# Optimization experiments

Hardware: AMD Instinct MI355X
Metric: run time of the kernel (lower is better)

## Reference

```python
import jax, jax.numpy as jnp
import numpy as np

B, N, F = 4096, 128, 3
EPS = 1e-5


def _bn(x, g, b):
    # BatchNorm1d(element_num) on [B, N, C]: channels are dim 1 (the N elements);
    # training-mode stats over dims (0, 2), biased variance (torch default).
    m = x.mean(axis=(0, 2), keepdims=True)
    v = ((x - m) ** 2).mean(axis=(0, 2), keepdims=True)
    return (x - m) / jnp.sqrt(v + EPS) * g[None, :, None] + b[None, :, None]


def _rel(x, W, bvec, psi, phi, wr):
    # f'_i = wr/N * sum_{j != i} (psi*phi * <x_i, x_j>) * relu(unary(x_j))
    n = x.shape[1]
    U = jax.nn.relu(jnp.einsum('bnd,ed->bne', x, W) + bvec)       # [B,N,D]
    S = (psi * phi) * jnp.einsum('bnd,bmd->bnm', x, x)            # [B,N,N]
    S = S * (1.0 - jnp.eye(n, dtype=x.dtype))                     # exclude j == i
    return wr * jnp.einsum('bnm,bmd->bnd', S, U) / n


def setup_inputs() -> dict:
    key = jax.random.key(0)
    ks = iter(jax.random.split(key, 64))
    d1, d2 = 2 * F, 4 * F  # 6, 12

    def w(shape, s=0.1):
        return (jax.random.normal(next(ks), shape, dtype=jnp.float32) * s)

    def scalar():
        return jax.random.uniform(next(ks), (), dtype=jnp.float32)

    inp = {
        'x': jax.random.normal(next(ks), (B, N, F), dtype=jnp.float32),
        'fc1_w': w((d1, F)), 'fc1_b': w((d1,)),
        'bn1_g': jnp.ones((N,), jnp.float32), 'bn1_b': jnp.zeros((N,), jnp.float32),
        'fc2_w': w((d2, d1)), 'fc2_b': w((d2,)),
        'bn2_g': jnp.ones((N,), jnp.float32), 'bn2_b': jnp.zeros((N,), jnp.float32),
        'fc3_w': w((d2, d2)), 'fc3_b': w((d2,)),
        'u1_w': w((d2, d2)), 'u1_b': w((d2,)), 'ps1': scalar(), 'ph1': scalar(), 'wr1': scalar(),
        'u2_w': w((d2, d2)), 'u2_b': w((d2,)), 'ps2': scalar(), 'ph2': scalar(), 'wr2': scalar(),
        'u3_w': w((d2, d2)), 'u3_b': w((d2,)), 'ps3': scalar(), 'ph3': scalar(), 'wr3': scalar(),
        'u4_w': w((d2, d2)), 'u4_b': w((d2,)), 'ps4': scalar(), 'ph4': scalar(), 'wr4': scalar(),
        'fc4_w': w((d1, d2)), 'fc4_b': w((d1,)),
        'bn4_g': jnp.ones((N,), jnp.float32), 'bn4_b': jnp.zeros((N,), jnp.float32),
        'fc5_w': w((F, d1)), 'fc5_b': w((F,)),
        'fc6_w': w((1, F)), 'fc6_b': w((1,)),
        'fc7_w': w((F - 1, F)), 'fc7_b': w((F - 1,)),
        'fc8_w': w((1, F)), 'fc8_b': w((1,)),
    }
    return inp


def reference(x, fc1_w, fc1_b, bn1_g, bn1_b, fc2_w, fc2_b, bn2_g, bn2_b,
              fc3_w, fc3_b,
              u1_w, u1_b, ps1, ph1, wr1,
              u2_w, u2_b, ps2, ph2, wr2,
              u3_w, u3_b, ps3, ph3, wr3,
              u4_w, u4_b, ps4, ph4, wr4,
              fc4_w, fc4_b, bn4_g, bn4_b,
              fc5_w, fc5_b, fc6_w, fc6_b, fc7_w, fc7_b, fc8_w, fc8_b):
    h = jax.nn.relu(_bn(jnp.einsum('bnf,ef->bne', x, fc1_w) + fc1_b, bn1_g, bn1_b))
    h = jax.nn.relu(_bn(jnp.einsum('bnf,ef->bne', h, fc2_w) + fc2_b, bn2_g, bn2_b))
    h = jax.nn.sigmoid(jnp.einsum('bnf,ef->bne', h, fc3_w) + fc3_b)
    h = _rel(h, u1_w, u1_b, ps1, ph1, wr1)
    h = _rel(h, u2_w, u2_b, ps2, ph2, wr2)
    h = _rel(h, u3_w, u3_b, ps3, ph3, wr3)
    h = _rel(h, u4_w, u4_b, ps4, ph4, wr4)
    h = jax.nn.relu(_bn(jnp.einsum('bnf,ef->bne', h, fc4_w) + fc4_b, bn4_g, bn4_b))
    h = jax.nn.relu(jnp.einsum('bnf,ef->bne', h, fc5_w) + fc5_b)
    cls = jnp.einsum('bnf,ef->bne', h, fc6_w) + fc6_b          # [B,N,1]
    geo = jnp.einsum('bnf,ef->bne', h, fc7_w) + fc7_b          # [B,N,F-1]
    res = jnp.concatenate([cls, geo], axis=2)                   # [B,N,F]
    pres = res.max(axis=1)                                      # MaxPool1d over all N -> [B,F]
    pred = jax.nn.sigmoid(pres @ fc8_w.T + fc8_b)               # [B,1]
    return pred
```

## Files before the change

### kernel.cpp

```cpp
#include <hip/hip_runtime.h>
#include <hip/hip_fp16.h>
#include <hip/hip_cooperative_groups.h>

namespace cg = cooperative_groups;

#define BB 4096
#define NN 128
#define EPS 1e-5f

#define S1 0
#define S2 2048
#define S4 4096
#define A4_OFF 6144

static __device__ __forceinline__ float sigmoidf_(float z){
  return 1.f/(1.f+__expf(-z));
}
static __device__ __forceinline__ float2 h2f2_(unsigned u){
  __half2 h = *reinterpret_cast<__half2*>(&u);
  return __half22float2(h);
}

static __device__ __forceinline__ float fdot2_(unsigned a, unsigned b, float c){
#if defined(__has_builtin)
#if __has_builtin(__builtin_amdgcn_fdot2)
  typedef _Float16 h2v __attribute__((ext_vector_type(2)));
  h2v av = *reinterpret_cast<h2v*>(&a);
  h2v bv = *reinterpret_cast<h2v*>(&b);
  return __builtin_amdgcn_fdot2(av, bv, c, false);
#else
  float2 af = h2f2_(a), bf = h2f2_(b);
  return fmaf(af.y, bf.y, fmaf(af.x, bf.x, c));
#endif
#else
  float2 af = h2f2_(a), bf = h2f2_(b);
  return fmaf(af.y, bf.y, fmaf(af.x, bf.x, c));
#endif
}

__global__ __launch_bounds__(256, 4) void kf(
  const float* __restrict__ x,
  const float* __restrict__ w1, const float* __restrict__ b1,
  const float* __restrict__ g1, const float* __restrict__ bb1,
  const float* __restrict__ w2, const float* __restrict__ b2,
  const float* __restrict__ g2, const float* __restrict__ bb2,
  const float* __restrict__ w3, const float* __restrict__ b3,
  const float* __restrict__ u1w, const float* __restrict__ u1b,
  const float* __restrict__ ps1, const float* __restrict__ ph1, const float* __restrict__ wr1,
  const float* __restrict__ u2w, const float* __restrict__ u2b,
  const float* __restrict__ ps2, const float* __restrict__ ph2, const float* __restrict__ wr2,
  const float* __restrict__ u3w, const float* __restrict__ u3b,
  const float* __restrict__ ps3, const float* __restrict__ ph3, const float* __restrict__ wr3,
  const float* __restrict__ u4w, const float* __restrict__ u4b,
  const float* __restrict__ ps4, const float* __restrict__ ph4, const float* __restrict__ wr4,
  const float* __restrict__ w4, const float* __restrict__ b4,
  const float* __restrict__ g4, const float* __restrict__ bb4,
  const float* __restrict__ w5, const float* __restrict__ b5,
  const float* __restrict__ w6, const float* __restrict__ b6,
  const float* __restrict__ w7, const float* __restrict__ b7,
  const float* __restrict__ w8, const float* __restrict__ b8,
  float* __restrict__ st, float* __restrict__ out)
{
  cg::grid_group grid = cg::this_grid();
  __shared__ float lds[4][1536];
  const int t = threadIdx.x;
  const int wave = t >> 6, lane = t & 63;
  const int b = blockIdx.x*4 + wave;
  const int r0 = lane*2, r1 = r0+1;
  const int shadow = (blockIdx.x & 7)*256;
  unsigned* Xp = (unsigned*)&lds[wave][0];
  unsigned* Up = (unsigned*)&lds[wave][768];

  const float2* xr = (const float2*)(x + ((size_t)b*128 + r0)*3);
  float2 c0=xr[0], c1=xr[1], c2=xr[2];
  const float xa0=c0.x, xa1=c0.y, xa2=c1.x;
  const float xb0=c1.y, xb1=c2.x, xb2=c2.y;

  float a6a[6], a6b[6];
  {
    float s0=0.f,q0=0.f,s1v=0.f,q1=0.f;
    #pragma unroll
    for (int e=0;e<6;e++){
      float va = fmaf(xa0,w1[e*3+0], fmaf(xa1,w1[e*3+1], fmaf(xa2,w1[e*3+2], b1[e])));
      float vb = fmaf(xb0,w1[e*3+0], fmaf(xb1,w1[e*3+1], fmaf(xb2,w1[e*3+2], b1[e])));
      a6a[e]=va; a6b[e]=vb;
      s0+=va; q0=fmaf(va,va,q0);
      s1v+=vb; q1=fmaf(vb,vb,q1);
    }
    lds[wave][r0]=s0; lds[wave][r1]=s1v;
    lds[wave][128+r0]=q0; lds[wave][128+r1]=q1;
    __syncthreads();
    atomicAdd(&st[S1 + shadow + t], lds[0][t]+lds[1][t]+lds[2][t]+lds[3][t]);
  }
  grid.sync();

  float z0[12], z1[12];
  {
    float sa=0.f,qa=0.f,sb=0.f,qb=0.f;
    #pragma unroll
    for (int c=0;c<8;c++){
      sa+=st[S1+c*256+r0]; qa+=st[S1+c*256+128+r0];
      sb+=st[S1+c*256+r1]; qb+=st[S1+c*256+128+r1];
    }
    const float inv1 = 1.f/(BB*6);
    float m=sa*inv1, v=qa*inv1-m*m;
    const float sA0=g1[r0]*rsqrtf(v+EPS), hA0=bb1[r0]-m*sA0;
    m=sb*inv1; v=qb*inv1-m*m;
    const float sA1=g1[r1]*rsqrtf(v+EPS), hA1=bb1[r1]-m*sA1;

    float h0[6], h1[6];
    #pragma unroll
    for (int e=0;e<6;e++){
      h0[e]=fmaxf(fmaf(a6a[e],sA0,hA0),0.f);
      h1[e]=fmaxf(fmaf(a6b[e],sA1,hA1),0.f);
    }
    float s0=0.f,q0=0.f,s1v=0.f,q1=0.f;
    #pragma unroll
    for (int d=0;d<12;d++){
      float za=b2[d], zb=b2[d];
      #pragma unroll
      for (int e=0;e<6;e++){ za=fmaf(h0[e],w2[d*6+e],za); zb=fmaf(h1[e],w2[d*6+e],zb); }
      z0[d]=za; z1[d]=zb;
      s0+=za; q0=fmaf(za,za,q0);
      s1v+=zb; q1=fmaf(zb,zb,q1);
    }
    lds[wave][r0]=s0; lds[wave][r1]=s1v;
    lds[wave][128+r0]=q0; lds[wave][128+r1]=q1;
    __syncthreads();
    atomicAdd(&st[S2 + shadow + t], lds[0][t]+lds[1][t]+lds[2][t]+lds[3][t]);
  }
  grid.sync();

  float X0[12], X1[12];
  {
    float sa=0.f,qa=0.f,sb=0.f,qb=0.f;
    #pragma unroll
    for (int c=0;c<8;c++){
      sa+=st[S2+c*256+r0]; qa+=st[S2+c*256+128+r0];
      sb+=st[S2+c*256+r1]; qb+=st[S2+c*256+128+r1];
    }
    const float inv2 = 1.f/(BB*12);
    float m=sa*inv2, v=qa*inv2-m*m;
    const float sB0=g2[r0]*rsqrtf(v+EPS), hB0=bb2[r0]-m*sB0;
    m=sb*inv2; v=qb*inv2-m*m;
    const float sB1=g2[r1]*rsqrtf(v+EPS), hB1=bb2[r1]-m*sB1;

    float h0[12], h1[12];
    #pragma unroll
    for (int d=0;d<12;d++){
      h0[d]=fmaxf(fmaf(z0[d],sB0,hB0),0.f);
      h1[d]=fmaxf(fmaf(z1[d],sB1,hB1),0.f);
    }
    #pragma unroll
    for (int d=0;d<12;d++){
      float za=b3[d], zb=b3[d];
      #pragma unroll
      for (int e=0;e<12;e++){ za=fmaf(h0[e],w3[d*12+e],za); zb=fmaf(h1[e],w3[d*12+e],zb); }
      X0[d]=sigmoidf_(za); X1[d]=sigmoidf_(zb);
    }
  }

  const float* UW[4]  = {u1w,u2w,u3w,u4w};
  const float* UBv[4] = {u1b,u2b,u3b,u4b};
  const float cf[4] = {
    wr1[0]*ps1[0]*ph1[0]*(1.f/128.f),
    wr2[0]*ps2[0]*ph2[0]*(1.f/128.f),
    wr3[0]*ps3[0]*ph3[0]*(1.f/128.f),
    wr4[0]*ps4[0]*ph4[0]*(1.f/128.f)
  };

  const int g = lane>>4;
  int kc = lane & 15; if (kc>11) kc=11;

  #pragma unroll
  for (int l=0;l<4;l++){
    const float* uw = UW[l];
    const float* ub = UBv[l];
    const float coef = cf[l];
    float Y0[12], Y1[12];
    {
      float U0[12], U1[12];
      #pragma unroll
      for (int d=0;d<12;d++){
        float za=ub[d], zb=ub[d];
        #pragma unroll
        for (int e=0;e<12;e++){ za=fmaf(X0[e],uw[d*12+e],za); zb=fmaf(X1[e],uw[d*12+e],zb); }
        U0[d]=fmaxf(za,0.f); U1[d]=fmaxf(zb,0.f);
      }
      float q0=0.f, q1=0.f;
      #pragma unroll
      for (int e=0;e<12;e++){ q0=fmaf(X0[e],X0[e],q0); q1=fmaf(X1[e],X1[e],q1); }
      __half2 hp[12], up[12];
      #pragma unroll
      for (int e=0;e<12;e++){
        hp[e] = __floats2half2_rn(X0[e],X1[e]);
        up[e] = __floats2half2_rn(U0[e],U1[e]);
      }
      {
        const uint4* hpv = (const uint4*)hp;
        const uint4* upv = (const uint4*)up;
        uint4* xw  = (uint4*)(Xp + lane*12);
        uint4* uwp = (uint4*)(Up + lane*12);
        xw[0]=hpv[0]; xw[1]=hpv[1]; xw[2]=hpv[2];
        uwp[0]=upv[0]; uwp[1]=upv[1]; uwp[2]=upv[2];
      }
      const float q0c = coef*q0, q1c = coef*q1;
      #pragma unroll
      for (int d=0;d<12;d++){ Y0[d] = -q0c*U0[d]; Y1[d] = -q1c*U1[d]; }
    }

    float mp[12];
    #pragma unroll
    for (int d=0;d<12;d++) mp[d]=0.f;
    #pragma unroll
    for (int i=0;i<16;i++){
      const int p = (g<<4) | ((i+g)&15);
      const unsigned xv2 = Xp[p*12 + kc];
      const uint4* urow = (const uint4*)(Up + p*12);
      uint4 ua=urow[0], ub4=urow[1], uc=urow[2];
      mp[0]=fdot2_(xv2, ua.x, mp[0]);  mp[1]=fdot2_(xv2, ua.y, mp[1]);
      mp[2]=fdot2_(xv2, ua.z, mp[2]);  mp[3]=fdot2_(xv2, ua.w, mp[3]);
      mp[4]=fdot2_(xv2, ub4.x, mp[4]); mp[5]=fdot2_(xv2, ub4.y, mp[5]);
      mp[6]=fdot2_(xv2, ub4.z, mp[6]); mp[7]=fdot2_(xv2, ub4.w, mp[7]);
      mp[8]=fdot2_(xv2, uc.x, mp[8]);  mp[9]=fdot2_(xv2, uc.y, mp[9]);
      mp[10]=fdot2_(xv2, uc.z, mp[10]); mp[11]=fdot2_(xv2, uc.w, mp[11]);
    }
    #pragma unroll
    for (int d=0;d<12;d++) mp[d] += __shfl_xor(mp[d], 16, 64);
    #pragma unroll
    for (int d=0;d<12;d++) mp[d] += __shfl_xor(mp[d], 32, 64);
    #pragma unroll
    for (int d=0;d<12;d++) mp[d] *= coef;

    #pragma unroll
    for (int k=0;k<12;k++){
      const float xa = X0[k], xb = X1[k];
      #pragma unroll
      for (int d=0;d<12;d++){
        const float mv = __int_as_float(__builtin_amdgcn_readlane(__float_as_int(mp[d]), k));
        Y0[d]=fmaf(xa,mv,Y0[d]); Y1[d]=fmaf(xb,mv,Y1[d]);
      }
    }
    #pragma unroll
    for (int d=0;d<12;d++){ X0[d]=Y0[d]; X1[d]=Y1[d]; }
  }

  float z4a[6], z4b[6];
  {
    float s0=0.f,q0=0.f,s1v=0.f,q1=0.f;
    #pragma unroll
    for (int e=0;e<6;e++){
      float a0=b4[e], a1v=b4[e];
      #pragma unroll
      for (int d=0;d<12;d++){ a0=fmaf(X0[d],w4[e*12+d],a0); a1v=fmaf(X1[d],w4[e*12+d],a1v); }
      z4a[e]=a0; z4b[e]=a1v;
      s0+=a0; q0=fmaf(a0,a0,q0);
      s1v+=a1v; q1=fmaf(a1v,a1v,q1);
    }
    __syncthreads();
    lds[wave][r0]=s0; lds[wave][r1]=s1v;
    lds[wave][128+r0]=q0; lds[wave][128+r1]=q1;
    __syncthreads();
    atomicAdd(&st[S4 + shadow + t], lds[0][t]+lds[1][t]+lds[2][t]+lds[3][t]);
  }
  grid.sync();

  {
    float ss0=0.f,qq0=0.f,ss1=0.f,qq1=0.f;
    #pragma unroll
    for (int cc=0;cc<8;cc++){
      ss0+=st[S4+cc*256+r0]; qq0+=st[S4+cc*256+128+r0];
      ss1+=st[S4+cc*256+r1]; qq1+=st[S4+cc*256+128+r1];
    }
    const float inv = 1.f/(BB*6);
    const float mean0=ss0*inv, var0=qq0*inv-mean0*mean0;
    const float sc0=g4[r0]*rsqrtf(var0+EPS), sh0=bb4[r0]-mean0*sc0;
    const float mean1=ss1*inv, var1=qq1*inv-mean1*mean1;
    const float sc1=g4[r1]*rsqrtf(var1+EPS), sh1=bb4[r1]-mean1*sc1;

    float h0[6], h1[6];
    #pragma unroll
    for (int e=0;e<6;e++){
      h0[e]=fmaxf(fmaf(z4a[e],sc0,sh0),0.f);
      h1[e]=fmaxf(fmaf(z4b[e],sc1,sh1),0.f);
    }
    float mx[3];
    {
      float h5a[3], h5b[3];
      #pragma unroll
      for (int f=0;f<3;f++){
        float za=b5[f], zb=b5[f];
        #pragma unroll
        for (int e=0;e<6;e++){ za=fmaf(h0[e],w5[f*6+e],za); zb=fmaf(h1[e],w5[f*6+e],zb); }
        h5a[f]=fmaxf(za,0.f); h5b[f]=fmaxf(zb,0.f);
      }
      float ca=b6[0], cb=b6[0];
      float g0a=b7[0], g0b=b7[0], g1a=b7[1], g1b=b7[1];
      #pragma unroll
      for (int f=0;f<3;f++){
        ca=fmaf(h5a[f],w6[f],ca);   cb=fmaf(h5b[f],w6[f],cb);
        g0a=fmaf(h5a[f],w7[f],g0a); g0b=fmaf(h5b[f],w7[f],g0b);
        g1a=fmaf(h5a[f],w7[3+f],g1a); g1b=fmaf(h5b[f],w7[3+f],g1b);
      }
      mx[0]=fmaxf(ca,cb); mx[1]=fmaxf(g0a,g0b); mx[2]=fmaxf(g1a,g1b);
    }
    #pragma unroll
    for (int off=32; off>0; off>>=1){
      mx[0]=fmaxf(mx[0], __shfl_xor(mx[0],off,64));
      mx[1]=fmaxf(mx[1], __shfl_xor(mx[1],off,64));
      mx[2]=fmaxf(mx[2], __shfl_xor(mx[2],off,64));
    }
    if (lane==0){
      float z = b8[0] + mx[0]*w8[0] + mx[1]*w8[1] + mx[2]*w8[2];
      out[b]=sigmoidf_(z);
    }
  }
}


__global__ __launch_bounds__(256) void k1(const float* __restrict__ x, const float* __restrict__ w1,
                   const float* __restrict__ b1, float* __restrict__ st){
  __shared__ float bl[512];
  const int t = threadIdx.x;
  const int tid = blockIdx.x*256 + t;
  float W[18], Bv[6];
  #pragma unroll
  for (int i=0;i<18;i++) W[i]=w1[i];
  #pragma unroll
  for (int i=0;i<6;i++) Bv[i]=b1[i];
  float s=0.f, sq=0.f;
  #pragma unroll
  for (int kk=0;kk<2;kk++){
    const int r = tid + kk*262144;
    const float* xr = x + (size_t)r*3;
    float x0=xr[0], x1=xr[1], x2=xr[2];
    #pragma unroll
    for (int e=0;e<6;e++){
      float a = fmaf(x0,W[e*3+0], fmaf(x1,W[e*3+1], fmaf(x2,W[e*3+2], Bv[e])));
      s+=a; sq=fmaf(a,a,sq);
    }
  }
  bl[t]=s; bl[256+t]=sq;
  __syncthreads();
  const int shadow = (blockIdx.x & 7)*256;
  if (t<128) atomicAdd(&st[S1+shadow+t], bl[t]+bl[t+128]);
  else       atomicAdd(&st[S1+shadow+t], bl[t+128]+bl[t+256]);
}

__global__ __launch_bounds__(256) void k2(const float* __restrict__ x,
                   const float* __restrict__ w1, const float* __restrict__ b1,
                   const float* __restrict__ g1, const float* __restrict__ bb1,
                   const float* __restrict__ w2, const float* __restrict__ b2,
                   float* __restrict__ st){
  __shared__ float bl[512];
  const int t = threadIdx.x;
  const int tid = blockIdx.x*256 + t;
  const int n = t & 127;
  float ss=0.f, qs=0.f;
  #pragma unroll
  for (int c=0;c<8;c++){ ss+=st[S1+c*256+n]; qs+=st[S1+c*256+128+n]; }
  const float mean = ss*(1.f/(BB*6));
  const float var  = qs*(1.f/(BB*6)) - mean*mean;
  const float sc = g1[n]*rsqrtf(var+EPS), sh = bb1[n]-mean*sc;
  float W1[18], B1v[6], W2[72], B2v[12];
  #pragma unroll
  for (int i=0;i<18;i++) W1[i]=w1[i];
  #pragma unroll
  for (int i=0;i<6;i++) B1v[i]=b1[i];
  #pragma unroll
  for (int i=0;i<72;i++) W2[i]=w2[i];
  #pragma unroll
  for (int i=0;i<12;i++) B2v[i]=b2[i];
  float s=0.f, sq=0.f;
  #pragma unroll
  for (int kk=0;kk<2;kk++){
    const int r = tid + kk*262144;
    const float* xr = x + (size_t)r*3;
    float x0=xr[0], x1=xr[1], x2=xr[2];
    float h[6];
    #pragma unroll
    for (int e=0;e<6;e++){
      float a = fmaf(x0,W1[e*3+0], fmaf(x1,W1[e*3+1], fmaf(x2,W1[e*3+2], B1v[e])));
      h[e]=fmaxf(fmaf(a,sc,sh),0.f);
    }
    #pragma unroll
    for (int d=0;d<12;d++){
      float z=B2v[d];
      #pragma unroll
      for (int e=0;e<6;e++) z=fmaf(h[e],W2[d*6+e],z);
      s+=z; sq=fmaf(z,z,sq);
    }
  }
  bl[t]=s; bl[256+t]=sq;
  __syncthreads();
  const int shadow = (blockIdx.x & 7)*256;
  if (t<128) atomicAdd(&st[S2+shadow+t], bl[t]+bl[t+128]);
  else       atomicAdd(&st[S2+shadow+t], bl[t+128]+bl[t+256]);
}

__global__ __launch_bounds__(256) void k3(
  const float* __restrict__ x,
  const float* __restrict__ w1, const float* __restrict__ b1,
  const float* __restrict__ g1, const float* __restrict__ bb1,
  const float* __restrict__ w2, const float* __restrict__ b2,
  const float* __restrict__ g2, const float* __restrict__ bb2,
  const float* __restrict__ w3, const float* __restrict__ b3,
  const float* __restrict__ u1w, const float* __restrict__ u1b,
  const float* __restrict__ ps1, const float* __restrict__ ph1, const float* __restrict__ wr1,
  const float* __restrict__ u2w, const float* __restrict__ u2b,
  const float* __restrict__ ps2, const float* __restrict__ ph2, const float* __restrict__ wr2,
  const float* __restrict__ u3w, const float* __restrict__ u3b,
  const float* __restrict__ ps3, const float* __restrict__ ph3, const float* __restrict__ wr3,
  const float* __restrict__ u4w, const float* __restrict__ u4b,
  const float* __restrict__ ps4, const float* __restrict__ ph4, const float* __restrict__ wr4,
  const float* __restrict__ w4, const float* __restrict__ b4,
  __half* __restrict__ a4, float* __restrict__ st)
{
  __shared__ float lds[4][1536];
  const int wave = threadIdx.x >> 6;
  const int lane = threadIdx.x & 63;
  const int b = blockIdx.x*4 + wave;
  unsigned* Xp = (unsigned*)&lds[wave][0];
  unsigned* Up = (unsigned*)&lds[wave][768];
  const int r0 = lane*2, r1 = r0+1;

  float s1a=0,q1a=0,s1b=0,q1b=0,s2a=0,q2a=0,s2b=0,q2b=0;
  #pragma unroll
  for (int c=0;c<8;c++){
    s1a+=st[S1+c*256+r0]; q1a+=st[S1+c*256+128+r0];
    s1b+=st[S1+c*256+r1]; q1b+=st[S1+c*256+128+r1];
    s2a+=st[S2+c*256+r0]; q2a+=st[S2+c*256+128+r0];
    s2b+=st[S2+c*256+r1]; q2b+=st[S2+c*256+128+r1];
  }
  const float inv1 = 1.f/(BB*6), inv2 = 1.f/(BB*12);
  float m = s1a*inv1, v = q1a*inv1 - m*m;
  const float sA0 = g1[r0]*rsqrtf(v+EPS), hA0 = bb1[r0]-m*sA0;
  m = s1b*inv1; v = q1b*inv1 - m*m;
  const float sA1 = g1[r1]*rsqrtf(v+EPS), hA1 = bb1[r1]-m*sA1;
  m = s2a*inv2; v = q2a*inv2 - m*m;
  const float sB0 = g2[r0]*rsqrtf(v+EPS), hB0 = bb2[r0]-m*sB0;
  m = s2b*inv2; v = q2b*inv2 - m*m;
  const float sB1 = g2[r1]*rsqrtf(v+EPS), hB1 = bb2[r1]-m*sB1;

  const float2* xr = (const float2*)(x + ((size_t)b*128 + r0)*3);
  float2 c0=xr[0], c1=xr[1], c2=xr[2];
  const float xa0=c0.x, xa1=c0.y, xa2=c1.x;
  const float xb0=c1.y, xb1=c2.x, xb2=c2.y;

  float X0[12], X1[12];
  {
    float g6a[6], g6b[6];
    #pragma unroll
    for (int e=0;e<6;e++){
      float a0 = fmaf(xa0,w1[e*3+0], fmaf(xa1,w1[e*3+1], fmaf(xa2,w1[e*3+2], b1[e])));
      float a1v= fmaf(xb0,w1[e*3+0], fmaf(xb1,w1[e*3+1], fmaf(xb2,w1[e*3+2], b1[e])));
      g6a[e]=fmaxf(fmaf(a0,sA0,hA0),0.f);
      g6b[e]=fmaxf(fmaf(a1v,sA1,hA1),0.f);
    }
    float h0[12], h1[12];
    #pragma unroll
    for (int d=0;d<12;d++){
      float z0=b2[d], z1=b2[d];
      #pragma unroll
      for (int e=0;e<6;e++){ z0=fmaf(g6a[e],w2[d*6+e],z0); z1=fmaf(g6b[e],w2[d*6+e],z1); }
      h0[d]=fmaxf(fmaf(z0,sB0,hB0),0.f);
      h1[d]=fmaxf(fmaf(z1,sB1,hB1),0.f);
    }
    #pragma unroll
    for (int d=0; d<12; d++){
      float z0=b3[d], z1=b3[d];
      #pragma unroll
      for (int e=0;e<12;e++){ z0=fmaf(h0[e],w3[d*12+e],z0); z1=fmaf(h1[e],w3[d*12+e],z1); }
      X0[d]=sigmoidf_(z0); X1[d]=sigmoidf_(z1);
    }
  }

  const float* UW[4]  = {u1w,u2w,u3w,u4w};
  const float* UBv[4] = {u1b,u2b,u3b,u4b};
  const float cf[4] = {
    wr1[0]*ps1[0]*ph1[0]*(1.f/128.f),
    wr2[0]*ps2[0]*ph2[0]*(1.f/128.f),
    wr3[0]*ps3[0]*ph3[0]*(1.f/128.f),
    wr4[0]*ps4[0]*ph4[0]*(1.f/128.f)
  };

  const int g = lane>>4;
  int kc = lane & 15; if (kc>11) kc=11;

  #pragma unroll
  for (int l=0;l<4;l++){
    const float* uw = UW[l];
    const float* ub = UBv[l];
    const float coef = cf[l];
    float Y0[12], Y1[12];
    {
      float U0[12], U1[12];
      #pragma unroll
      for (int d=0;d<12;d++){
        float z0=ub[d], z1=ub[d];
        #pragma unroll
        for (int e=0;e<12;e++){ z0=fmaf(X0[e],uw[d*12+e],z0); z1=fmaf(X1[e],uw[d*12+e],z1); }
        U0[d]=fmaxf(z0,0.f); U1[d]=fmaxf(z1,0.f);
      }
      float q0=0.f, q1=0.f;
      #pragma unroll
      for (int e=0;e<12;e++){ q0=fmaf(X0[e],X0[e],q0); q1=fmaf(X1[e],X1[e],q1); }
      __half2 hp[12], up[12];
      #pragma unroll
      for (int e=0;e<12;e++){
        hp[e] = __floats2half2_rn(X0[e],X1[e]);
        up[e] = __floats2half2_rn(U0[e],U1[e]);
      }
      {
        const uint4* hpv = (const uint4*)hp;
        const uint4* upv = (const uint4*)up;
        uint4* xw = (uint4*)(Xp + lane*12);
        uint4* uwp = (uint4*)(Up + lane*12);
        xw[0]=hpv[0]; xw[1]=hpv[1]; xw[2]=hpv[2];
        uwp[0]=upv[0]; uwp[1]=upv[1]; uwp[2]=upv[2];
      }
      const float q0c = coef*q0, q1c = coef*q1;
      #pragma unroll
      for (int d=0;d<12;d++){ Y0[d] = -q0c*U0[d]; Y1[d] = -q1c*U1[d]; }
    }

    float mp[12];
    #pragma unroll
    for (int d=0;d<12;d++) mp[d]=0.f;
    #pragma unroll
    for (int i=0;i<16;i++){
      const int p = (g<<4) | ((i+g)&15);
      const unsigned xv2 = Xp[p*12 + kc];
      const uint4* urow = (const uint4*)(Up + p*12);
      uint4 ua=urow[0], ub4=urow[1], uc=urow[2];
      mp[0]=fdot2_(xv2, ua.x, mp[0]);  mp[1]=fdot2_(xv2, ua.y, mp[1]);
      mp[2]=fdot2_(xv2, ua.z, mp[2]);  mp[3]=fdot2_(xv2, ua.w, mp[3]);
      mp[4]=fdot2_(xv2, ub4.x, mp[4]); mp[5]=fdot2_(xv2, ub4.y, mp[5]);
      mp[6]=fdot2_(xv2, ub4.z, mp[6]); mp[7]=fdot2_(xv2, ub4.w, mp[7]);
      mp[8]=fdot2_(xv2, uc.x, mp[8]);  mp[9]=fdot2_(xv2, uc.y, mp[9]);
      mp[10]=fdot2_(xv2, uc.z, mp[10]); mp[11]=fdot2_(xv2, uc.w, mp[11]);
    }
    #pragma unroll
    for (int d=0;d<12;d++) mp[d] += __shfl_xor(mp[d], 16, 64);
    #pragma unroll
    for (int d=0;d<12;d++) mp[d] += __shfl_xor(mp[d], 32, 64);
    #pragma unroll
    for (int d=0;d<12;d++) mp[d] *= coef;

    #pragma unroll
    for (int k=0;k<12;k++){
      const float xa = X0[k], xb = X1[k];
      #pragma unroll
      for (int d=0;d<12;d++){
        const float mv = __int_as_float(__builtin_amdgcn_readlane(__float_as_int(mp[d]), k));
        Y0[d]=fmaf(xa,mv,Y0[d]); Y1[d]=fmaf(xb,mv,Y1[d]);
      }
    }
    #pragma unroll
    for (int d=0;d<12;d++){ X0[d]=Y0[d]; X1[d]=Y1[d]; }
  }

  float z0[6], z1[6];
  float s0=0.f,sq0=0.f,s1=0.f,sq1=0.f;
  #pragma unroll
  for (int e=0;e<6;e++){
    float a0=b4[e], a1v=b4[e];
    #pragma unroll
    for (int d=0;d<12;d++){ a0=fmaf(X0[d],w4[e*12+d],a0); a1v=fmaf(X1[d],w4[e*12+d],a1v); }
    z0[e]=a0; z1[e]=a1v;
    s0+=a0; sq0=fmaf(a0,a0,sq0); s1+=a1v; sq1=fmaf(a1v,a1v,sq1);
  }
  {
    __half2 ha[6];
    ha[0]=__floats2half2_rn(z0[0],z0[1]); ha[1]=__floats2half2_rn(z0[2],z0[3]); ha[2]=__floats2half2_rn(z0[4],z0[5]);
    ha[3]=__floats2half2_rn(z1[0],z1[1]); ha[4]=__floats2half2_rn(z1[2],z1[3]); ha[5]=__floats2half2_rn(z1[4],z1[5]);
    const uint2* hv = (const uint2*)ha;
    uint2* aw = (uint2*)(a4 + ((size_t)b*128 + r0)*6);
    aw[0]=hv[0]; aw[1]=hv[1]; aw[2]=hv[2];
  }

  __syncthreads();
  lds[wave][r0]=s0; lds[wave][r1]=s1;
  lds[wave][128+r0]=sq0; lds[wave][128+r1]=sq1;
  __syncthreads();
  const int t = threadIdx.x;
  const int c = (blockIdx.x & 7)*256;
  atomicAdd(&st[S4 + c + t], lds[0][t]+lds[1][t]+lds[2][t]+lds[3][t]);
}

__global__ __launch_bounds__(256) void k4(
  const __half* __restrict__ a4, const float* __restrict__ g4, const float* __restrict__ bb4,
  const float* __restrict__ w5, const float* __restrict__ b5,
  const float* __restrict__ w6, const float* __restrict__ b6,
  const float* __restrict__ w7, const float* __restrict__ b7,
  const float* __restrict__ w8, const float* __restrict__ b8,
  const float* __restrict__ st, float* __restrict__ out)
{
  const int wave = threadIdx.x>>6, lane = threadIdx.x&63;
  const int b = blockIdx.x*4 + wave;
  const int r0 = lane*2, r1 = r0+1;
  float ss0=0.f, qq0=0.f, ss1=0.f, qq1=0.f;
  #pragma unroll
  for (int cc=0;cc<8;cc++){
    ss0 += st[S4+cc*256+r0];     qq0 += st[S4+cc*256+128+r0];
    ss1 += st[S4+cc*256+r1];     qq1 += st[S4+cc*256+128+r1];
  }
  const float inv = 1.f/(BB*6);
  const float mean0 = ss0*inv, var0 = qq0*inv - mean0*mean0;
  const float sc0 = g4[r0]*rsqrtf(var0+EPS), sh0 = bb4[r0]-mean0*sc0;
  const float mean1 = ss1*inv, var1 = qq1*inv - mean1*mean1;
  const float sc1 = g4[r1]*rsqrtf(var1+EPS), sh1 = bb4[r1]-mean1*sc1;

  const uint2* ar = (const uint2*)(a4 + ((size_t)b*128 + r0)*6);
  uint2 v0=ar[0], v1=ar[1], v2=ar[2];
  float2 f0=h2f2_(v0.x), f1=h2f2_(v0.y), f2=h2f2_(v1.x);
  float2 f3=h2f2_(v1.y), f4=h2f2_(v2.x), f5=h2f2_(v2.y);
  float h0[6] = {f0.x,f0.y,f1.x,f1.y,f2.x,f2.y};
  float h1[6] = {f3.x,f3.y,f4.x,f4.y,f5.x,f5.y};
  #pragma unroll
  for (int e=0;e<6;e++){
    h0[e]=fmaxf(fmaf(h0[e],sc0,sh0),0.f);
    h1[e]=fmaxf(fmaf(h1[e],sc1,sh1),0.f);
  }
  float mx[3];
  {
    float h5a[3], h5b[3];
    #pragma unroll
    for (int f=0;f<3;f++){
      float za=b5[f], zb=b5[f];
      #pragma unroll
      for (int e=0;e<6;e++){ za=fmaf(h0[e],w5[f*6+e],za); zb=fmaf(h1[e],w5[f*6+e],zb); }
      h5a[f]=fmaxf(za,0.f); h5b[f]=fmaxf(zb,0.f);
    }
    float ca=b6[0], cb=b6[0];
    float g0a=b7[0], g0b=b7[0], g1a=b7[1], g1b=b7[1];
    #pragma unroll
    for (int f=0;f<3;f++){
      ca=fmaf(h5a[f],w6[f],ca);   cb=fmaf(h5b[f],w6[f],cb);
      g0a=fmaf(h5a[f],w7[f],g0a); g0b=fmaf(h5b[f],w7[f],g0b);
      g1a=fmaf(h5a[f],w7[3+f],g1a); g1b=fmaf(h5b[f],w7[3+f],g1b);
    }
    mx[0]=fmaxf(ca,cb); mx[1]=fmaxf(g0a,g0b); mx[2]=fmaxf(g1a,g1b);
  }
  #pragma unroll
  for (int off=32; off>0; off>>=1){
    mx[0]=fmaxf(mx[0], __shfl_xor(mx[0],off,64));
    mx[1]=fmaxf(mx[1], __shfl_xor(mx[1],off,64));
    mx[2]=fmaxf(mx[2], __shfl_xor(mx[2],off,64));
  }
  if (lane==0){
    float z = b8[0] + mx[0]*w8[0] + mx[1]*w8[1] + mx[2]*w8[2];
    out[b]=sigmoidf_(z);
  }
}

extern "C" void kernel_launch(void* const* d_in, const int* in_sizes, int n_in,
                              void* d_out, int out_size, void* d_ws, size_t ws_size,
                              hipStream_t stream){
  const float* x   = (const float*)d_in[0];
  const float* f1w = (const float*)d_in[1];
  const float* f1b = (const float*)d_in[2];
  const float* g1  = (const float*)d_in[3];
  const float* bb1 = (const float*)d_in[4];
  const float* f2w = (const float*)d_in[5];
  const float* f2b = (const float*)d_in[6];
  const float* g2  = (const float*)d_in[7];
  const float* bb2 = (const float*)d_in[8];
  const float* f3w = (const float*)d_in[9];
  const float* f3b = (const float*)d_in[10];
  const float* u1w = (const float*)d_in[11];
  const float* u1b = (const float*)d_in[12];
  const float* ps1 = (const float*)d_in[13];
  const float* ph1 = (const float*)d_in[14];
  const float* wr1 = (const float*)d_in[15];
  const float* u2w = (const float*)d_in[16];
  const float* u2b = (const float*)d_in[17];
  const float* ps2 = (const float*)d_in[18];
  const float* ph2 = (const float*)d_in[19];
  const float* wr2 = (const float*)d_in[20];
  const float* u3w = (const float*)d_in[21];
  const float* u3b = (const float*)d_in[22];
  const float* ps3 = (const float*)d_in[23];
  const float* ph3 = (const float*)d_in[24];
  const float* wr3 = (const float*)d_in[25];
  const float* u4w = (const float*)d_in[26];
  const float* u4b = (const float*)d_in[27];
  const float* ps4 = (const float*)d_in[28];
  const float* ph4 = (const float*)d_in[29];
  const float* wr4 = (const float*)d_in[30];
  const float* f4w = (const float*)d_in[31];
  const float* f4b = (const float*)d_in[32];
  const float* g4  = (const float*)d_in[33];
  const float* bb4 = (const float*)d_in[34];
  const float* f5w = (const float*)d_in[35];
  const float* f5b = (const float*)d_in[36];
  const float* f6w = (const float*)d_in[37];
  const float* f6b = (const float*)d_in[38];
  const float* f7w = (const float*)d_in[39];
  const float* f7b = (const float*)d_in[40];
  const float* f8w = (const float*)d_in[41];
  const float* f8b = (const float*)d_in[42];

  float* wsf = (float*)d_ws;
  float* st  = wsf;
  __half* a4 = (__half*)(wsf + A4_OFF);
  float* out = (float*)d_out;

  static int coop_ok = 1;
  if (coop_ok){
    void* args[] = {
      (void*)&x,
      (void*)&f1w, (void*)&f1b, (void*)&g1,  (void*)&bb1,
      (void*)&f2w, (void*)&f2b, (void*)&g2,  (void*)&bb2,
      (void*)&f3w, (void*)&f3b,
      (void*)&u1w, (void*)&u1b, (void*)&ps1, (void*)&ph1, (void*)&wr1,
      (void*)&u2w, (void*)&u2b, (void*)&ps2, (void*)&ph2, (void*)&wr2,
      (void*)&u3w, (void*)&u3b, (void*)&ps3, (void*)&ph3, (void*)&wr3,
      (void*)&u4w, (void*)&u4b, (void*)&ps4, (void*)&ph4, (void*)&wr4,
      (void*)&f4w, (void*)&f4b, (void*)&g4,  (void*)&bb4,
      (void*)&f5w, (void*)&f5b, (void*)&f6w, (void*)&f6b,
      (void*)&f7w, (void*)&f7b, (void*)&f8w, (void*)&f8b,
      (void*)&st, (void*)&out
    };
    hipError_t e = hipLaunchCooperativeKernel((const void*)kf, dim3(1024), dim3(256),
                                              args, 0, stream);
    if (e != hipSuccess){
      coop_ok = 0;
      (void)hipGetLastError();
    }
  }
  if (!coop_ok){
    k1<<<dim3(1024), dim3(256), 0, stream>>>(x, f1w, f1b, st);
    k2<<<dim3(1024), dim3(256), 0, stream>>>(x, f1w, f1b, g1, bb1, f2w, f2b, st);
    k3<<<dim3(1024), dim3(256), 0, stream>>>(x, f1w, f1b, g1, bb1, f2w, f2b, g2, bb2,
        f3w, f3b,
        u1w,u1b,ps1,ph1,wr1, u2w,u2b,ps2,ph2,wr2,
        u3w,u3b,ps3,ph3,wr3, u4w,u4b,ps4,ph4,wr4,
        f4w, f4b, a4, st);
    k4<<<dim3(1024), dim3(256), 0, stream>>>(a4, g4, bb4, f5w, f5b,
        f6w, f6b, f7w, f7b, f8w, f8b, st, out);
  }
}
```

Measured before the change: 197.7 us.

## Replace cooperative grid.sync with custom hierarchical atomic grid barrier

```diff
diff --git a/kernel.cpp b/kernel.cpp
--- a/kernel.cpp
+++ b/kernel.cpp
@@ -1,8 +1,5 @@
 #include <hip/hip_runtime.h>
 #include <hip/hip_fp16.h>
-#include <hip/hip_cooperative_groups.h>
-
-namespace cg = cooperative_groups;
 
 #define BB 4096
 #define NN 128
@@ -36,6 +33,28 @@
   float2 af = h2f2_(a), bf = h2f2_(b);
   return fmaf(af.y, bf.y, fmaf(af.x, bf.x, c));
 #endif
+}
+
+static __device__ __forceinline__ float cload_f(const float* p){
+  return __hip_atomic_load(p, __ATOMIC_RELAXED, __HIP_MEMORY_SCOPE_AGENT);
+}
+static __device__ __forceinline__ int cload_i(const int* p){
+  return __hip_atomic_load(p, __ATOMIC_RELAXED, __HIP_MEMORY_SCOPE_AGENT);
+}
+
+static __device__ __forceinline__ void gbar(int* __restrict__ bar, int phase){
+  __syncthreads();
+  if (threadIdx.x == 0){
+    int* base = bar + phase*2048;
+    int* grp  = base + (blockIdx.x & 63)*16;
+    int* root = base + 1024;
+    int old = __hip_atomic_fetch_add(grp, 1, __ATOMIC_RELAXED, __HIP_MEMORY_SCOPE_AGENT);
+    if (old == 15)
+      __hip_atomic_fetch_add(root, 1, __ATOMIC_RELAXED, __HIP_MEMORY_SCOPE_AGENT);
+    while (cload_i(root) < 64)
+      __builtin_amdgcn_s_sleep(2);
+  }
+  __syncthreads();
 }
 
 __global__ __launch_bounds__(256, 4) void kf(
@@ -59,10 +78,10 @@
   const float* __restrict__ w6, const float* __restrict__ b6,
   const float* __restrict__ w7, const float* __restrict__ b7,
   const float* __restrict__ w8, const float* __restrict__ b8,
-  float* __restrict__ st, float* __restrict__ out)
+  float* __restrict__ st, int* __restrict__ bar, float* __restrict__ out)
 {
-  cg::grid_group grid = cg::this_grid();
   __shared__ float lds[4][1536];
+  __shared__ float stg[256];
   const int t = threadIdx.x;
   const int wave = t >> 6, lane = t & 63;
   const int b = blockIdx.x*4 + wave;
@@ -92,20 +111,19 @@
     __syncthreads();
     atomicAdd(&st[S1 + shadow + t], lds[0][t]+lds[1][t]+lds[2][t]+lds[3][t]);
   }
-  grid.sync();
+  gbar(bar, 0);
 
   float z0[12], z1[12];
   {
-    float sa=0.f,qa=0.f,sb=0.f,qb=0.f;
-    #pragma unroll
-    for (int c=0;c<8;c++){
-      sa+=st[S1+c*256+r0]; qa+=st[S1+c*256+128+r0];
-      sb+=st[S1+c*256+r1]; qb+=st[S1+c*256+128+r1];
-    }
+    float acc=0.f;
+    #pragma unroll
+    for (int c=0;c<8;c++) acc += cload_f(&st[S1 + c*256 + t]);
+    stg[t]=acc;
+    __syncthreads();
     const float inv1 = 1.f/(BB*6);
-    float m=sa*inv1, v=qa*inv1-m*m;
+    float m=stg[r0]*inv1, v=stg[128+r0]*inv1-m*m;
     const float sA0=g1[r0]*rsqrtf(v+EPS), hA0=bb1[r0]-m*sA0;
-    m=sb*inv1; v=qb*inv1-m*m;
+    m=stg[r1]*inv1; v=stg[128+r1]*inv1-m*m;
     const float sA1=g1[r1]*rsqrtf(v+EPS), hA1=bb1[r1]-m*sA1;
 
     float h0[6], h1[6];
@@ -124,25 +142,25 @@
       s0+=za; q0=fmaf(za,za,q0);
       s1v+=zb; q1=fmaf(zb,zb,q1);
     }
+    __syncthreads();
     lds[wave][r0]=s0; lds[wave][r1]=s1v;
     lds[wave][128+r0]=q0; lds[wave][128+r1]=q1;
     __syncthreads();
     atomicAdd(&st[S2 + shadow + t], lds[0][t]+lds[1][t]+lds[2][t]+lds[3][t]);
   }
-  grid.sync();
+  gbar(bar, 1);
 
   float X0[12], X1[12];
   {
-    float sa=0.f,qa=0.f,sb=0.f,qb=0.f;
-    #pragma unroll
-    for (int c=0;c<8;c++){
-      sa+=st[S2+c*256+r0]; qa+=st[S2+c*256+128+r0];
-      sb+=st[S2+c*256+r1]; qb+=st[S2+c*256+128+r1];
-    }
+    float acc=0.f;
+    #pragma unroll
+    for (int c=0;c<8;c++) acc += cload_f(&st[S2 + c*256 + t]);
+    stg[t]=acc;
+    __syncthreads();
     const float inv2 = 1.f/(BB*12);
-    float m=sa*inv2, v=qa*inv2-m*m;
+    float m=stg[r0]*inv2, v=stg[128+r0]*inv2-m*m;
     const float sB0=g2[r0]*rsqrtf(v+EPS), hB0=bb2[r0]-m*sB0;
-    m=sb*inv2; v=qb*inv2-m*m;
+    m=stg[r1]*inv2; v=stg[128+r1]*inv2-m*m;
     const float sB1=g2[r1]*rsqrtf(v+EPS), hB1=bb2[r1]-m*sB1;
 
     float h0[12], h1[12];
@@ -263,19 +281,18 @@
     __syncthreads();
     atomicAdd(&st[S4 + shadow + t], lds[0][t]+lds[1][t]+lds[2][t]+lds[3][t]);
   }
-  grid.sync();
+  gbar(bar, 2);
 
   {
-    float ss0=0.f,qq0=0.f,ss1=0.f,qq1=0.f;
-    #pragma unroll
-    for (int cc=0;cc<8;cc++){
-      ss0+=st[S4+cc*256+r0]; qq0+=st[S4+cc*256+128+r0];
-      ss1+=st[S4+cc*256+r1]; qq1+=st[S4+cc*256+128+r1];
-    }
+    float acc=0.f;
+    #pragma unroll
+    for (int c=0;c<8;c++) acc += cload_f(&st[S4 + c*256 + t]);
+    stg[t]=acc;
+    __syncthreads();
     const float inv = 1.f/(BB*6);
-    const float mean0=ss0*inv, var0=qq0*inv-mean0*mean0;
+    const float mean0=stg[r0]*inv, var0=stg[128+r0]*inv-mean0*mean0;
     const float sc0=g4[r0]*rsqrtf(var0+EPS), sh0=bb4[r0]-mean0*sc0;
-    const float mean1=ss1*inv, var1=qq1*inv-mean1*mean1;
+    const float mean1=stg[r1]*inv, var1=stg[128+r1]*inv-mean1*mean1;
     const float sc1=g4[r1]*rsqrtf(var1+EPS), sh1=bb4[r1]-mean1*sc1;
 
     float h0[6], h1[6];
@@ -703,10 +720,15 @@
 
   float* wsf = (float*)d_ws;
   float* st  = wsf;
+  int*   bar = (int*)(wsf + A4_OFF);
   __half* a4 = (__half*)(wsf + A4_OFF);
   float* out = (float*)d_out;
 
   static int coop_ok = 1;
+  if (coop_ok){
+    hipError_t em = hipMemsetAsync(bar, 0, 3*2048*sizeof(int), stream);
+    if (em != hipSuccess){ coop_ok = 0; (void)hipGetLastError(); }
+  }
   if (coop_ok){
     void* args[] = {
       (void*)&x,
@@ -720,7 +742,7 @@
       (void*)&f4w, (void*)&f4b, (void*)&g4,  (void*)&bb4,
       (void*)&f5w, (void*)&f5b, (void*)&f6w, (void*)&f6b,
       (void*)&f7w, (void*)&f7b, (void*)&f8w, (void*)&f8b,
-      (void*)&st, (void*)&out
+      (void*)&st, (void*)&bar, (void*)&out
     };
     hipError_t e = hipLaunchCooperativeKernel((const void*)kf, dim3(1024), dim3(256),
                                               args, 0, stream);
```

Result: no change. 199.0 us (+0.7%).
